# Performance work log

Hardware: AMD Instinct MI355X
Metric: run time of the kernel (lower is better)

The kernel has to match this reference:

```python
import jax, jax.numpy as jnp
import numpy as np

N = 100000      # nodes
E = 1600000     # edges
F_IN = 256      # input features
H = 128         # hidden_dim
C = 40          # num_classes
L = 4           # num_layers
STEP = 0.1


def setup_inputs() -> dict:
    key = jax.random.key(0)
    ks = jax.random.split(key, 8)
    s = 0.05
    return {
        "x": jax.random.normal(ks[0], (N, F_IN), jnp.float32),
        "edge_index": jax.random.randint(ks[1], (2, E), 0, N),
        "enc_W": jax.random.normal(ks[2], (H, F_IN), jnp.float32) * s,
        "enc_b": jnp.zeros((H,), jnp.float32),
        "W_raw": jax.random.normal(ks[3], (L, H, H + 2), jnp.float32) * s,
        "W_b": jnp.zeros((L, H), jnp.float32),
        "ext_w": jax.random.normal(ks[4], (L, H), jnp.float32),
        "beta": jax.random.normal(ks[5], (L,), jnp.float32),
        "dec_W": jax.random.normal(ks[6], (C, H), jnp.float32) * s,
        "dec_b": jnp.zeros((C,), jnp.float32),
    }


def _pairwise_weight(Wr):
    # Wr: (H, H+2) raw weight -> symmetric effective weight (H, H)
    W0 = jnp.triu(Wr[:, :-2], 1)
    W0 = W0 + W0.T
    diag = Wr[:, -2] * jnp.sum(jnp.abs(W0), axis=1) + Wr[:, -1]
    return W0 + jnp.diag(diag)


def reference(x, edge_index, enc_W, enc_b, W_raw, W_b, ext_w, beta, dec_W, dec_b):
    row, col = edge_index[0], edge_index[1]
    n = x.shape[0]
    # degree over source nodes (edge_index[0]), recomputed identically each layer
    deg = jnp.zeros((n,), x.dtype).at[row].add(jnp.float32(1.0))
    deg_inv = jnp.where(deg > 0, jnp.where(deg > 0, deg, 1.0) ** -0.5, 0.0)
    # message = deg_inv[row]*deg_inv[col] * x_i (x_i = features of target col),
    # scatter-added at target col  ==>  per-node coefficient times node feature
    coef = jnp.zeros((n,), x.dtype).at[col].add(deg_inv[row] * deg_inv[col])

    h = x @ enc_W.T + enc_b
    h0 = h
    for l in range(W_raw.shape[0]):
        W_eff = _pairwise_weight(W_raw[l])        # symmetric (H,H)
        out_p = h @ W_eff.T + W_b[l]              # pairwise linear transform
        agg = coef[:, None] * out_p               # gather+normalize+scatter-add
        out = agg - (h * ext_w[l][None, :] + beta[l] * h0)
        h = h + STEP * jax.nn.relu(out)
    return h @ dec_W.T + dec_b
```

## Files before the change

### kernel.cpp

```cpp
#include <hip/hip_runtime.h>

typedef unsigned int u32;
typedef unsigned short u16;
typedef __bf16 bf16x8 __attribute__((ext_vector_type(8)));
typedef float f32x16 __attribute__((ext_vector_type(16)));
typedef u32 u32x4 __attribute__((ext_vector_type(4)));

#define HDIM 128
#define FIN  256
#define NCLS 40
#define NL   4
#define BN   16384
#define NSL  32

__device__ __forceinline__ u16 f2b(float f){
  union { __bf16 h; u16 s; } u; u.h = (__bf16)f; return u.s;
}
__device__ __forceinline__ u32 pk(float a, float b){
  union { __bf16 h[2]; u32 w; } u; u.h[0] = (__bf16)a; u.h[1] = (__bf16)b; return u.w;
}
__device__ __forceinline__ float ubf(u32 hbits){
  union { u32 w; float f; } u; u.w = hbits << 16; return u.f;
}
__device__ __forceinline__ float dinv(float d){ return d > 0.f ? rsqrtf(d) : 0.f; }

__device__ __forceinline__ int fragIdx128(int row, int k){
  return (((((row >> 5) * 8 + (k >> 4)) * 2 + ((k >> 3) & 1)) * 32 + (row & 31)) * 8) + (k & 7);
}
__device__ __forceinline__ int fragIdx64(int row, int k){
  return (((((row >> 5) * 4 + (k >> 4)) * 2 + ((k >> 3) & 1)) * 32 + (row & 31)) * 8) + (k & 7);
}

__global__ void prep_kernel(const float* __restrict__ encW, const float* __restrict__ Wraw,
                            const float* __restrict__ decW,
                            u16* __restrict__ encF, u16* __restrict__ weffF, u16* __restrict__ decB){
  int b = blockIdx.x, t = threadIdx.x;
  if(b < 512){
    int i = b * 64 + t;
    int row = i >> 8, k = i & 255;
    int chunk = k >> 6, kk = k & 63;
    encF[chunk * 8192 + fragIdx64(row, kk)] = f2b(encW[i]);
  } else if(b < 1024){
    int idx = b - 512;
    int l = idx >> 7, i = idx & 127;
    const float* Wr = Wraw + (size_t)l * HDIM * (HDIM + 2);
    float w0a, w0b, s = 0.f;
    { int j = t;
      float v = (i < j) ? Wr[i*(HDIM+2)+j] : ((j < i) ? Wr[j*(HDIM+2)+i] : 0.f);
      w0a = v; s += fabsf(v); }
    { int j = t + 64;
      float v = (i < j) ? Wr[i*(HDIM+2)+j] : ((j < i) ? Wr[j*(HDIM+2)+i] : 0.f);
      w0b = v; s += fabsf(v); }
    #pragma unroll
    for(int d = 1; d < 64; d <<= 1) s += __shfl_xor(s, d, 64);
    float diag = Wr[i*(HDIM+2)+HDIM] * s + Wr[i*(HDIM+2)+HDIM+1];
    u16* o = weffF + (size_t)l * 16384;
    o[fragIdx128(i, t)]      = f2b((t == i)      ? diag : w0a);
    o[fragIdx128(i, t + 64)] = f2b((t + 64 == i) ? diag : w0b);
  } else {
    int idx = b - 1024;
    int i = idx * 64 + t;
    int c = i >> 7, k = i & 127;
    decB[i] = (c < NCLS) ? f2b(decW[c * HDIM + k]) : (u16)0;
  }
}


template<int WEIGHTED>
__global__ void __launch_bounds__(256, 2)
hist_kernel(const int* __restrict__ idx, const int* __restrict__ src,
            const float* __restrict__ dv, float* __restrict__ partial,
            int E, int Nn, int NB, int chunk)
{
  __shared__ float buck[BN];
  const int tid = threadIdx.x;
  const int g = blockIdx.x % NB;
  const int s = blockIdx.x / NB;
  const int lo = g << 14;

  for(int i = tid; i < BN; i += 256) buck[i] = 0.f;
  __syncthreads();

  long e0 = (long)s * chunk;
  long e1 = (long)E < e0 + chunk ? (long)E : e0 + chunk;
  if(e0 < e1){
    long ng = (e1 - e0) >> 2;
    for(long gi = tid; gi < ng; gi += 256){
      long e = e0 + gi * 4;
      int4 c = *(const int4*)(idx + e);
      int4 r;
      if(WEIGHTED) r = *(const int4*)(src + e);
      int k;
      k = c.x - lo; if((u32)k < (u32)BN) atomicAdd(&buck[k], WEIGHTED ? dv[r.x] : 1.f);
      k = c.y - lo; if((u32)k < (u32)BN) atomicAdd(&buck[k], WEIGHTED ? dv[r.y] : 1.f);
      k = c.z - lo; if((u32)k < (u32)BN) atomicAdd(&buck[k], WEIGHTED ? dv[r.z] : 1.f);
      k = c.w - lo; if((u32)k < (u32)BN) atomicAdd(&buck[k], WEIGHTED ? dv[r.w] : 1.f);
    }
    long et = e0 + ng * 4;
    if(et + tid < e1){
      long e = et + tid;
      int k = idx[e] - lo;
      if((u32)k < (u32)BN) atomicAdd(&buck[k], WEIGHTED ? dv[src[e]] : 1.f);
    }
  }
  __syncthreads();

  float* dst = partial + (size_t)s * ((size_t)NB << 14) + lo;
  int hi = Nn - lo < BN ? Nn - lo : BN;
  for(int i = tid; i < hi; i += 256) dst[i] = buck[i];
}

template<int MODE>
__global__ void reduce_kernel(const float* __restrict__ partial, const float* __restrict__ dvin,
                              float* __restrict__ outv, int Nn, int NB, int S)
{
  int i = blockIdx.x * 256 + threadIdx.x;
  if(i >= Nn) return;
  const size_t NnPad = (size_t)NB << 14;
  float t = 0.f;
  for(int s = 0; s < S; s++) t += partial[(size_t)s * NnPad + i];
  outv[i] = MODE ? dvin[i] * t : (t > 0.f ? rsqrtf(t) : 0.f);
}


__global__ void deg_kernel(const int* __restrict__ ei, float* __restrict__ deg, int E){
  long e = ((long)blockIdx.x * 256 + threadIdx.x) * 8;
  if(e + 7 < E){
    int4 v0 = *(const int4*)(ei + e);
    int4 v1 = *(const int4*)(ei + e + 4);
    atomicAdd(&deg[v0.x], 1.0f); atomicAdd(&deg[v0.y], 1.0f);
    atomicAdd(&deg[v0.z], 1.0f); atomicAdd(&deg[v0.w], 1.0f);
    atomicAdd(&deg[v1.x], 1.0f); atomicAdd(&deg[v1.y], 1.0f);
    atomicAdd(&deg[v1.z], 1.0f); atomicAdd(&deg[v1.w], 1.0f);
  } else {
    for(; e < E; e++) atomicAdd(&deg[ei[e]], 1.0f);
  }
}

__global__ void coef_kernel(const int* __restrict__ ei, const float* __restrict__ deg,
                            float* __restrict__ coef, int E){
  long e = ((long)blockIdx.x * 256 + threadIdx.x) * 8;
  if(e + 7 < E){
    int4 r0 = *(const int4*)(ei + e);
    int4 r1 = *(const int4*)(ei + e + 4);
    int4 c0 = *(const int4*)(ei + E + e);
    int4 c1 = *(const int4*)(ei + E + e + 4);
    atomicAdd(&coef[c0.x], dinv(deg[r0.x]) * dinv(deg[c0.x]));
    atomicAdd(&coef[c0.y], dinv(deg[r0.y]) * dinv(deg[c0.y]));
    atomicAdd(&coef[c0.z], dinv(deg[r0.z]) * dinv(deg[c0.z]));
    atomicAdd(&coef[c0.w], dinv(deg[r0.w]) * dinv(deg[c0.w]));
    atomicAdd(&coef[c1.x], dinv(deg[r1.x]) * dinv(deg[c1.x]));
    atomicAdd(&coef[c1.y], dinv(deg[r1.y]) * dinv(deg[c1.y]));
    atomicAdd(&coef[c1.z], dinv(deg[r1.z]) * dinv(deg[c1.z]));
    atomicAdd(&coef[c1.w], dinv(deg[r1.w]) * dinv(deg[c1.w]));
  } else {
    for(; e < E; e++){
      int r = ei[e], c = ei[E + e];
      atomicAdd(&coef[c], dinv(deg[r]) * dinv(deg[c]));
    }
  }
}

__device__ __forceinline__ bf16x8 buildBp(u32 P0, u32 P1, u32 P2, u32 P3, int hi){
  u32 S0 = hi ? P0 : P2;
  u32 S1 = hi ? P1 : P3;
  u32 R0 = __shfl_xor(S0, 32, 64);
  u32 R1 = __shfl_xor(S1, 32, 64);
  union { u32 w[4]; bf16x8 b; } u;
  u.w[0] = hi ? R0 : P0;
  u.w[1] = hi ? R1 : P1;
  u.w[2] = hi ? P2 : R0;
  u.w[3] = hi ? P3 : R1;
  return u.b;
}

__device__ __forceinline__ void stage32k(u16* __restrict__ lds, const u16* __restrict__ src, int tid){
  const u32x4* s = (const u32x4*)src;
  u32x4* d = (u32x4*)lds;
  #pragma unroll
  for(int i = 0; i < 8; i++) d[tid + i * 256] = s[tid + i * 256];
}

__global__ void __launch_bounds__(256, 2)
enc_kernel(const float* __restrict__ x, const float* __restrict__ enc_b,
           const u16* __restrict__ encF, u32* __restrict__ h0F, int Nn)
{
  __shared__ u16 lw[8192];
  __shared__ u16 xc[8192];

  const int tid  = threadIdx.x;
  const int lane = tid & 63;
  const int hi   = lane >> 5;
  const int ln   = lane & 31;
  const int nib  = (tid >> 6) * 32 + ln;
  const int blk  = blockIdx.x;

  f32x16 acc[4];
  #pragma unroll
  for(int nt = 0; nt < 4; nt++)
    #pragma unroll
    for(int i = 0; i < 16; i++) acc[nt][i] = 0.f;

  const int r0 = tid >> 4;
  const int c4 = (tid & 15) * 4;
  const int g  = c4 >> 3, j = c4 & 7;

  for(int chunk = 0; chunk < 4; chunk++){
    __syncthreads();
    {
      const u32x4* s = (const u32x4*)(encF + chunk * 8192);
      u32x4* d = (u32x4*)lw;
      #pragma unroll
      for(int i = 0; i < 4; i++) d[tid + i * 256] = s[tid + i * 256];
    }
    #pragma unroll
    for(int i = 0; i < 8; i++){
      int r = i * 16 + r0;
      int gn = blk * 128 + r; if(gn >= Nn) gn = Nn - 1;
      float4 v = *(const float4*)(x + (size_t)gn * FIN + chunk * 64 + c4);
      u32* d = (u32*)(xc + g * 1024 + ((r ^ (g & 7)) << 3) + j);
      d[0] = pk(v.x, v.y);
      d[1] = pk(v.z, v.w);
    }
    __syncthreads();

    #pragma unroll
    for(int ksl = 0; ksl < 4; ksl++){
      #pragma unroll
      for(int nt = 0; nt < 4; nt++){
        const int gg = ksl * 2 + hi;
        const bf16x8 B = *(const bf16x8*)(xc + gg * 1024 + ((nib ^ (gg & 7)) << 3));
        const bf16x8 A = *(const bf16x8*)(lw + ((((nt * 4 + ksl) * 2 + hi) * 32 + ln) * 8));
        acc[nt] = __builtin_amdgcn_mfma_f32_32x32x16_bf16(A, B, acc[nt], 0, 0, 0);
      }
    }
  }

  u32* dst = h0F + (size_t)blk * 8192;
  #pragma unroll
  for(int nt = 0; nt < 4; nt++){
    #pragma unroll
    for(int q = 0; q < 4; q++){
      float4 eb = *(const float4*)(enc_b + nt * 32 + 8 * q + 4 * hi);
      acc[nt][4*q+0] += eb.x; acc[nt][4*q+1] += eb.y;
      acc[nt][4*q+2] += eb.z; acc[nt][4*q+3] += eb.w;
    }
    #pragma unroll
    for(int m = 0; m < 8; m++)
      dst[(nt * 8 + m) * 256 + tid] = pk(acc[nt][2*m], acc[nt][2*m+1]);
  }
}

__global__ void __launch_bounds__(256, 2)
lay_kernel(const float* __restrict__ W_b, const float* __restrict__ ext_w,
           const float* __restrict__ beta, const float* __restrict__ dec_b,
           const float* __restrict__ coef, const u32* __restrict__ h0F,
           const u16* __restrict__ weffF, const u16* __restrict__ decB,
           float* __restrict__ out, int Nn)
{
  __shared__ u16 lw[16384];
  __shared__ u32 hns[16][256];

  const int tid  = threadIdx.x;
  const int lane = tid & 63;
  const int wv   = tid >> 6;
  const int hi   = lane >> 5;
  const int ln   = lane & 31;
  const int nib  = wv * 32 + ln;
  const int node = blockIdx.x * 128 + nib;
  const int nd   = node < Nn ? node : (Nn - 1);
  const float cf = coef[nd];

  u32 hp[32];
  const u32* srcH = h0F + (size_t)blockIdx.x * 8192;
  #pragma unroll
  for(int m = 0; m < 32; m++)
    hp[m] = srcH[m * 256 + tid];

  for(int l = 0; l < NL; l++){
    __syncthreads();
    stage32k(lw, weffF + l * 16384, tid);
    __syncthreads();

    const float bet = beta[l];

    #pragma unroll
    for(int P = 0; P < 2; P++){
      f32x16 a0, a1;
      #pragma unroll
      for(int i = 0; i < 16; i++){ a0[i] = 0.f; a1[i] = 0.f; }

      #pragma unroll
      for(int ks = 0; ks < 8; ks++){
        const int wbase = (ks >> 1) * 8 + 4 * (ks & 1);
        bf16x8 B = buildBp(hp[wbase+0], hp[wbase+1], hp[wbase+2], hp[wbase+3], hi);
        const bf16x8 A0 = *(const bf16x8*)(lw + (((((2*P+0) * 8 + ks) * 2 + hi) * 32 + ln) * 8));
        const bf16x8 A1 = *(const bf16x8*)(lw + (((((2*P+1) * 8 + ks) * 2 + hi) * 32 + ln) * 8));
        a0 = __builtin_amdgcn_mfma_f32_32x32x16_bf16(A0, B, a0, 0, 0, 0);
        a1 = __builtin_amdgcn_mfma_f32_32x32x16_bf16(A1, B, a1, 0, 0, 0);
      }

      #pragma unroll
      for(int t = 0; t < 2; t++){
        const int nt = 2*P + t;
        f32x16& a = t ? a1 : a0;
        #pragma unroll
        for(int q = 0; q < 4; q++){
          const int fb = nt * 32 + 8 * q + 4 * hi;
          float4 wb = *(const float4*)(W_b   + l * HDIM + fb);
          float4 ew = *(const float4*)(ext_w + l * HDIM + fb);
          #pragma unroll
          for(int r2 = 0; r2 < 4; r2++){
            const int r = 4 * q + r2;
            float wbv = (r2==0)?wb.x:(r2==1)?wb.y:(r2==2)?wb.z:wb.w;
            float ewv = (r2==0)?ew.x:(r2==1)?ew.y:(r2==2)?ew.z:ew.w;
            u32 w0 = srcH[(nt * 8 + (r >> 1)) * 256 + tid];
            u32 wc = hp[nt * 8 + (r >> 1)];
            float h0v = ubf((r & 1) ? (w0 >> 16) : (w0 & 0xffffu));
            float hv  = ubf((r & 1) ? (wc >> 16) : (wc & 0xffffu));
            float o = cf * (a[r] + wbv) - hv * ewv - bet * h0v;
            a[r] = hv + 0.1f * fmaxf(o, 0.f);
          }
        }
        #pragma unroll
        for(int m = 0; m < 8; m++){
          u32 w = pk(a[2*m], a[2*m+1]);
          if(P == 0) hns[nt * 8 + m][tid] = w;
          else       hp[nt * 8 + m] = w;
        }
      }
    }
    #pragma unroll
    for(int m = 0; m < 16; m++) hp[m] = hns[m][tid];
  }

  f32x16 d0, d1;
  #pragma unroll
  for(int i = 0; i < 16; i++){ d0[i] = 0.f; d1[i] = 0.f; }

  #pragma unroll
  for(int ks = 0; ks < 8; ks++){
    const int wbase = (ks >> 1) * 8 + 4 * (ks & 1);
    bf16x8 B = buildBp(hp[wbase+0], hp[wbase+1], hp[wbase+2], hp[wbase+3], hi);
    const bf16x8 A0 = *(const bf16x8*)(decB + (0 * 32 + ln) * HDIM + ks * 16 + hi * 8);
    const bf16x8 A1 = *(const bf16x8*)(decB + (1 * 32 + ln) * HDIM + ks * 16 + hi * 8);
    d0 = __builtin_amdgcn_mfma_f32_32x32x16_bf16(A0, B, d0, 0, 0, 0);
    d1 = __builtin_amdgcn_mfma_f32_32x32x16_bf16(A1, B, d1, 0, 0, 0);
  }

  if(node < Nn){
    #pragma unroll
    for(int nt = 0; nt < 2; nt++){
      const f32x16& d = nt ? d1 : d0;
      #pragma unroll
      for(int q = 0; q < 4; q++){
        if(nt == 0 || q == 0){
          const int c0 = nt * 32 + 8 * q + 4 * hi;
          float4 db = *(const float4*)(dec_b + c0);
          float4 v;
          v.x = d[4*q+0] + db.x;
          v.y = d[4*q+1] + db.y;
          v.z = d[4*q+2] + db.z;
          v.w = d[4*q+3] + db.w;
          *(float4*)(out + (size_t)node * NCLS + c0) = v;
        }
      }
    }
  }
}

extern "C" void kernel_launch(void* const* d_in, const int* in_sizes, int n_in,
                              void* d_out, int out_size, void* d_ws, size_t ws_size,
                              hipStream_t stream){
  (void)n_in; (void)out_size;
  const float* x     = (const float*)d_in[0];
  const int*   ei    = (const int*)  d_in[1];
  const float* encW  = (const float*)d_in[2];
  const float* enc_b = (const float*)d_in[3];
  const float* Wraw  = (const float*)d_in[4];
  const float* W_b   = (const float*)d_in[5];
  const float* ext_w = (const float*)d_in[6];
  const float* beta  = (const float*)d_in[7];
  const float* decW  = (const float*)d_in[8];
  const float* dec_b = (const float*)d_in[9];
  float* out = (float*)d_out;
  const int Nn = in_sizes[0] / FIN;
  const int E  = in_sizes[1] / 2;
  const int nBlk = (Nn + 127) / 128;
  const int NB   = (Nn + BN - 1) / BN;
  const int chunk = (((E + NSL - 1) / NSL) + 3) & ~3;

  char* ws = (char*)d_ws;
  size_t szN = ((size_t)Nn * 4 + 511) & ~(size_t)511;
  float* coef = (float*)(ws);
  float* dv   = (float*)(ws + szN);
  u16* encF   = (u16*)(ws + 2 * szN);
  u16* weffF  = (u16*)(ws + 2 * szN + 65536);
  u16* decB   = (u16*)(ws + 2 * szN + 65536 + 131072);
  u32* h0F    = (u32*)(ws + 2 * szN + 65536 + 131072 + 16384);
  float* partial = (float*)(ws + 2 * szN + 65536 + 131072 + 16384 + (size_t)nBlk * 32768);
  const size_t partialBytes = (size_t)NSL * ((size_t)NB << 14) * 4;
  const size_t need = 2 * szN + 65536 + 131072 + 16384 + (size_t)nBlk * 32768 + partialBytes;
  const bool fast = ws_size >= need;

  prep_kernel<<<1152, 64, 0, stream>>>(encW, Wraw, decW, encF, weffF, decB);
  const int ngrid = (Nn + 255) / 256;
  if(fast){
    hist_kernel<0><<<NB * NSL, 256, 0, stream>>>(ei, ei, dv, partial, E, Nn, NB, chunk);
    reduce_kernel<0><<<ngrid, 256, 0, stream>>>(partial, dv, dv, Nn, NB, NSL);
    hist_kernel<1><<<NB * NSL, 256, 0, stream>>>(ei + E, ei, dv, partial, E, Nn, NB, chunk);
    reduce_kernel<1><<<ngrid, 256, 0, stream>>>(partial, dv, coef, Nn, NB, NSL);
  } else {
    const int egrid = (int)((E / 8 + 255) / 256) + 1;
    hipMemsetAsync(ws, 0, 2 * szN, stream);
    deg_kernel <<<egrid, 256, 0, stream>>>(ei, dv, E);
    coef_kernel<<<egrid, 256, 0, stream>>>(ei, dv, coef, E);
  }
  enc_kernel <<<nBlk, 256, 0, stream>>>(x, enc_b, encF, h0F, Nn);
  lay_kernel <<<nBlk, 256, 0, stream>>>(W_b, ext_w, beta, dec_b, coef, h0F, weffF, decB, out, Nn);
}
```

Before: 196.8 us.

## Double-buffer layer weights with async global-to-LDS loads in layer kernel

Splits each layer's 32KB weight tile into two 16KB halves and double-buffers them in LDS. The next half is prefetched with global_load_lds while the MFMAs for the current half run, replacing the synchronous register-staged copy that was bracketed by two barriers. The encoder kernel also switches its weight staging to the async global-to-LDS path. The cost is one barrier per half-layer step and reliance on that barrier's implicit vmcnt wait for the async loads to finish.

```diff
diff --git a/kernel.cpp b/kernel.cpp
--- a/kernel.cpp
+++ b/kernel.cpp
@@ -29,6 +29,17 @@
 }
 __device__ __forceinline__ int fragIdx64(int row, int k){
   return (((((row >> 5) * 4 + (k >> 4)) * 2 + ((k >> 3) & 1)) * 32 + (row & 31)) * 8) + (k & 7);
+}
+
+__device__ __forceinline__ void stage16k_async(u16* lds, const u16* src, int wv, int lane){
+  #pragma unroll
+  for(int i = 0; i < 4; i++){
+    const int off = (wv * 4 + i) * 1024;
+    __builtin_amdgcn_global_load_lds(
+      (const __attribute__((address_space(1))) void*)((const char*)src + off + lane * 16),
+      (__attribute__((address_space(3))) void*)((char*)lds + off),
+      16, 0, 0);
+  }
 }
 
 __global__ void prep_kernel(const float* __restrict__ encW, const float* __restrict__ Wraw,
@@ -174,13 +185,6 @@
   return u.b;
 }
 
-__device__ __forceinline__ void stage32k(u16* __restrict__ lds, const u16* __restrict__ src, int tid){
-  const u32x4* s = (const u32x4*)src;
-  u32x4* d = (u32x4*)lds;
-  #pragma unroll
-  for(int i = 0; i < 8; i++) d[tid + i * 256] = s[tid + i * 256];
-}
-
 __global__ void __launch_bounds__(256, 2)
 enc_kernel(const float* __restrict__ x, const float* __restrict__ enc_b,
            const u16* __restrict__ encF, u32* __restrict__ h0F, int Nn)
@@ -190,9 +194,10 @@
 
   const int tid  = threadIdx.x;
   const int lane = tid & 63;
+  const int wv   = tid >> 6;
   const int hi   = lane >> 5;
   const int ln   = lane & 31;
-  const int nib  = (tid >> 6) * 32 + ln;
+  const int nib  = wv * 32 + ln;
   const int blk  = blockIdx.x;
 
   f32x16 acc[4];
@@ -207,12 +212,7 @@
 
   for(int chunk = 0; chunk < 4; chunk++){
     __syncthreads();
-    {
-      const u32x4* s = (const u32x4*)(encF + chunk * 8192);
-      u32x4* d = (u32x4*)lw;
-      #pragma unroll
-      for(int i = 0; i < 4; i++) d[tid + i * 256] = s[tid + i * 256];
-    }
+    stage16k_async(lw, encF + chunk * 8192, wv, lane);
     #pragma unroll
     for(int i = 0; i < 8; i++){
       int r = i * 16 + r0;
@@ -258,7 +258,7 @@
            const u16* __restrict__ weffF, const u16* __restrict__ decB,
            float* __restrict__ out, int Nn)
 {
-  __shared__ u16 lw[16384];
+  __shared__ u16 lw[2][8192];
   __shared__ u32 hns[16][256];
 
   const int tid  = threadIdx.x;
@@ -277,61 +277,66 @@
   for(int m = 0; m < 32; m++)
     hp[m] = srcH[m * 256 + tid];
 
-  for(int l = 0; l < NL; l++){
-    __syncthreads();
-    stage32k(lw, weffF + l * 16384, tid);
-    __syncthreads();
+  stage16k_async(lw[0], weffF, wv, lane);
+  __syncthreads();
+
+  #pragma unroll
+  for(int p = 0; p < 2 * NL; p++){
+    const int l = p >> 1, P = p & 1, cur = p & 1;
+
+    if(p < 2 * NL - 1)
+      stage16k_async(lw[cur ^ 1], weffF + ((p + 1) >> 1) * 16384 + ((p + 1) & 1) * 8192, wv, lane);
 
     const float bet = beta[l];
-
-    #pragma unroll
-    for(int P = 0; P < 2; P++){
-      f32x16 a0, a1;
+    f32x16 a0, a1;
+    #pragma unroll
+    for(int i = 0; i < 16; i++){ a0[i] = 0.f; a1[i] = 0.f; }
+
+    #pragma unroll
+    for(int ks = 0; ks < 8; ks++){
+      const int wbase = (ks >> 1) * 8 + 4 * (ks & 1);
+      bf16x8 B = buildBp(hp[wbase+0], hp[wbase+1], hp[wbase+2], hp[wbase+3], hi);
+      const bf16x8 A0 = *(const bf16x8*)(lw[cur] + ((((0 * 8 + ks) * 2 + hi) * 32 + ln) * 8));
+      const bf16x8 A1 = *(const bf16x8*)(lw[cur] + ((((1 * 8 + ks) * 2 + hi) * 32 + ln) * 8));
+      a0 = __builtin_amdgcn_mfma_f32_32x32x16_bf16(A0, B, a0, 0, 0, 0);
+      a1 = __builtin_amdgcn_mfma_f32_32x32x16_bf16(A1, B, a1, 0, 0, 0);
+    }
+
+    #pragma unroll
+    for(int t = 0; t < 2; t++){
+      const int nt = 2*P + t;
+      f32x16& a = t ? a1 : a0;
       #pragma unroll
-      for(int i = 0; i < 16; i++){ a0[i] = 0.f; a1[i] = 0.f; }
-
-      #pragma unroll
-      for(int ks = 0; ks < 8; ks++){
-        const int wbase = (ks >> 1) * 8 + 4 * (ks & 1);
-        bf16x8 B = buildBp(hp[wbase+0], hp[wbase+1], hp[wbase+2], hp[wbase+3], hi);
-        const bf16x8 A0 = *(const bf16x8*)(lw + (((((2*P+0) * 8 + ks) * 2 + hi) * 32 + ln) * 8));
-        const bf16x8 A1 = *(const bf16x8*)(lw + (((((2*P+1) * 8 + ks) * 2 + hi) * 32 + ln) * 8));
-        a0 = __builtin_amdgcn_mfma_f32_32x32x16_bf16(A0, B, a0, 0, 0, 0);
-        a1 = __builtin_amdgcn_mfma_f32_32x32x16_bf16(A1, B, a1, 0, 0, 0);
-      }
-
-      #pragma unroll
-      for(int t = 0; t < 2; t++){
-        const int nt = 2*P + t;
-        f32x16& a = t ? a1 : a0;
+      for(int q = 0; q < 4; q++){
+        const int fb = nt * 32 + 8 * q + 4 * hi;
+        float4 wb = *(const float4*)(W_b   + l * HDIM + fb);
+        float4 ew = *(const float4*)(ext_w + l * HDIM + fb);
         #pragma unroll
-        for(int q = 0; q < 4; q++){
-          const int fb = nt * 32 + 8 * q + 4 * hi;
-          float4 wb = *(const float4*)(W_b   + l * HDIM + fb);
-          float4 ew = *(const float4*)(ext_w + l * HDIM + fb);
-          #pragma unroll
-          for(int r2 = 0; r2 < 4; r2++){
-            const int r = 4 * q + r2;
-            float wbv = (r2==0)?wb.x:(r2==1)?wb.y:(r2==2)?wb.z:wb.w;
-            float ewv = (r2==0)?ew.x:(r2==1)?ew.y:(r2==2)?ew.z:ew.w;
-            u32 w0 = srcH[(nt * 8 + (r >> 1)) * 256 + tid];
-            u32 wc = hp[nt * 8 + (r >> 1)];
-            float h0v = ubf((r & 1) ? (w0 >> 16) : (w0 & 0xffffu));
-            float hv  = ubf((r & 1) ? (wc >> 16) : (wc & 0xffffu));
-            float o = cf * (a[r] + wbv) - hv * ewv - bet * h0v;
-            a[r] = hv + 0.1f * fmaxf(o, 0.f);
-          }
-        }
-        #pragma unroll
-        for(int m = 0; m < 8; m++){
-          u32 w = pk(a[2*m], a[2*m+1]);
-          if(P == 0) hns[nt * 8 + m][tid] = w;
-          else       hp[nt * 8 + m] = w;
+        for(int r2 = 0; r2 < 4; r2++){
+          const int r = 4 * q + r2;
+          float wbv = (r2==0)?wb.x:(r2==1)?wb.y:(r2==2)?wb.z:wb.w;
+          float ewv = (r2==0)?ew.x:(r2==1)?ew.y:(r2==2)?ew.z:ew.w;
+          u32 w0 = srcH[(nt * 8 + (r >> 1)) * 256 + tid];
+          u32 wc = hp[nt * 8 + (r >> 1)];
+          float h0v = ubf((r & 1) ? (w0 >> 16) : (w0 & 0xffffu));
+          float hv  = ubf((r & 1) ? (wc >> 16) : (wc & 0xffffu));
+          float o = cf * (a[r] + wbv) - hv * ewv - bet * h0v;
+          a[r] = hv + 0.1f * fmaxf(o, 0.f);
         }
       }
-    }
-    #pragma unroll
-    for(int m = 0; m < 16; m++) hp[m] = hns[m][tid];
+      #pragma unroll
+      for(int m = 0; m < 8; m++){
+        u32 w = pk(a[2*m], a[2*m+1]);
+        if(P == 0) hns[nt * 8 + m][tid] = w;
+        else       hp[nt * 8 + m] = w;
+      }
+    }
+    if(P == 1){
+      #pragma unroll
+      for(int m = 0; m < 16; m++) hp[m] = hns[m][tid];
+    }
+
+    __syncthreads();
   }
 
   f32x16 d0, d1;
```

Result: faster. 183.4 us (-6.8%).
